# Performance work log

Measured on AMD Instinct MI355X. Metric: run time of the kernel, lower is better.

## Reference

```python
import jax, jax.numpy as jnp
import numpy as np
from jax import lax

D = 2048; H = 32; N = 64; S = 2048
LW = 64; LA = 64; LG = 128; LV = 32


def _ln(z, w, b, eps):
    m = jnp.mean(z, axis=-1, keepdims=True)
    v = jnp.var(z, axis=-1, keepdims=True)
    return (z - m) * lax.rsqrt(v + eps) * w + b


def setup_inputs():
    ks = iter(jax.random.split(jax.random.key(0), 40))
    nrm = lambda shape, s=1.0: jax.random.normal(next(ks), shape, dtype=jnp.float32) * s
    return {
        "x": nrm((1, S, D)),
        "state1": nrm((D,)),
        "state2": nrm((H, N, N), 0.1),
        "v_first": nrm((S, H, N)),
        "ln1_w": jnp.ones((D,), jnp.float32),
        "ln1_b": jnp.zeros((D,), jnp.float32),
        "x_r": nrm((D,), 0.1), "x_w": nrm((D,), 0.1), "x_k": nrm((D,), 0.1),
        "x_v": nrm((D,), 0.1), "x_a": nrm((D,), 0.1), "x_g": nrm((D,), 0.1),
        "Wr": nrm((D, D), 0.02), "Wk": nrm((D, D), 0.02),
        "Wv": nrm((D, D), 0.02), "Wo": nrm((D, D), 0.02),
        "w1": nrm((D, LW), 0.02), "w2": nrm((LW, D), 0.05), "w0": nrm((D,), 0.1),
        "a1": nrm((D, LA), 0.02), "a2": nrm((LA, D), 0.05), "a0": nrm((D,), 0.1),
        "g1": nrm((D, LG), 0.02), "g2": nrm((LG, D), 0.05),
        "v1": nrm((D, LV), 0.02), "v2": nrm((LV, D), 0.05), "v0": nrm((D,), 0.1),
        "k_k": nrm((H, N), 0.5), "k_a": nrm((H, N), 0.5), "r_k": nrm((H, N), 0.5),
        "ln_x_w": jnp.ones((D,), jnp.float32),
        "ln_x_b": jnp.zeros((D,), jnp.float32),
    }


def _forward(x, state1, state2, v_first, ln1_w, ln1_b, x_r, x_w, x_k, x_v, x_a, x_g,
             Wr, Wk, Wv, Wo, w1, w2, w0, a1, a2, a0, g1, g2, v1, v2, v0,
             k_k, k_a, r_k, ln_x_w, ln_x_b):
    last_x = x
    xn = _ln(x, ln1_w, ln1_b, 1e-5)                      # (1,S,D)
    state1_out = xn[:, -1:]
    past = jnp.concatenate([state1.reshape(1, 1, D), xn[:, :-1]], axis=1)
    sx = past - xn                                        # token-shift delta
    xr = xn + sx * x_r; xw = xn + sx * x_w; xk = xn + sx * x_k
    xv = xn + sx * x_v; xa = xn + sx * x_a; xg = xn + sx * x_g
    r = (xr @ Wr.T).reshape(S, H, N)
    k = (xk @ Wk.T).reshape(S, H, N)
    v = (xv @ Wv.T).reshape(S, H, N)
    gate = jax.nn.sigmoid(xg @ g1) @ g2                   # (1,S,D)
    a = jax.nn.sigmoid((xa @ a1) @ a2 + a0).reshape(S, H, N)
    td = jnp.tanh(xw @ w1) @ w2 + w0
    w_dec = jnp.exp(-0.606531 * jax.nn.sigmoid(td)).reshape(S, H, N)
    kk = k * k_k
    kk = kk / jnp.maximum(jnp.linalg.norm(kk, axis=-1, keepdims=True), 1e-12)
    k = k * (1.0 + (a - 1.0) * k_a)
    # layer_id != 0: residual value mixing with v_first
    v = v + (v_first - v) * jax.nn.sigmoid(((xv @ v1) @ v2 + v0).reshape(S, H, N))
    b = kk * a
    a_neg = -kk

    def step(s, inp):
        # s: (H,N,N) state; each input (H,N)
        r_t, w_t, k_t, v_t, a_t, b_t = inp
        sa = jnp.einsum('hij,hj->hi', s, a_t)
        s = s * w_t[:, None, :] + sa[:, :, None] * b_t[:, None, :] + v_t[:, :, None] * k_t[:, None, :]
        return s, jnp.einsum('hij,hj->hi', s, r_t)

    state2_out, y = lax.scan(step, state2, (r, w_dec, k, v, a_neg, b))  # y: (S,H,N)
    o = _ln(y, 1.0, 0.0, 0.00064).reshape(1, S, D)       # ln_x (default affine)
    o = o * ln_x_w + ln_x_b
    rkv = (jnp.sum(r * k * r_k, axis=-1, keepdims=True) * v).reshape(1, S, D)
    o = (o + rkv) * gate
    o = o @ Wo.T
    return last_x + o, state1_out, state2_out


def reference(x, state1, state2, v_first, ln1_w, ln1_b, x_r, x_w, x_k, x_v, x_a, x_g,
              Wr, Wk, Wv, Wo, w1, w2, w0, a1, a2, a0, g1, g2, v1, v2, v0,
              k_k, k_a, r_k, ln_x_w, ln_x_b):
    return _forward(x, state1, state2, v_first, ln1_w, ln1_b, x_r, x_w, x_k, x_v, x_a, x_g,
                    Wr, Wk, Wv, Wo, w1, w2, w0, a1, a2, a0, g1, g2, v1, v2, v0,
                    k_k, k_a, r_k, ln_x_w, ln_x_b)
```

## Files before the change

kernel.cpp:

```cpp
#include <hip/hip_runtime.h>
#include <math.h>

#define kD 2048
#define kH 32
#define kN 64
#define kS 2048

typedef unsigned short ushort_t;
typedef unsigned int uint32;

__device__ __forceinline__ ushort_t f2bf(float f) {
  uint32 u = __float_as_uint(f);
  u += 0x7fffu + ((u >> 16) & 1u);
  return (ushort_t)(u >> 16);
}
__device__ __forceinline__ float bf2f(ushort_t u) {
  return __uint_as_float(((uint32)u) << 16);
}
__device__ __forceinline__ float sigm(float x) { return 1.f / (1.f + __expf(-x)); }

__global__ __launch_bounds__(256) void ln1_kernel(
    const float* __restrict__ x, const float* __restrict__ w, const float* __restrict__ b,
    ushort_t* __restrict__ xnbf, ushort_t* __restrict__ xprevbf,
    const float* __restrict__ state1, float* __restrict__ state1_out)
// ... 64 lines not shown

__global__ __launch_bounds__(256) void gemm_bf16_b(GemmArgs args)
{
  int z = blockIdx.z;
  const ushort_t* __restrict__ A = args.A[z];
  const ushort_t* __restrict__ B = args.B[z];
  float* __restrict__ C = args.C[z];
  const float* __restrict__ resid = args.resid[z];

  __shared__ __align__(16) ushort_t As[128 * 64];
  __shared__ __align__(16) ushort_t Bs[128 * 64];
  int tid = threadIdx.x;
  int w = tid >> 6, lane = tid & 63;
  int row0 = blockIdx.y * 128, col0 = blockIdx.x * 128;
  int wrow = (w >> 1) * 64, wcol = (w & 1) * 64;
  int quad = lane >> 4, r16 = lane & 15;
  f32x4 acc[4][4] = {};

  int lrow = lane >> 3;
  int lsw  = (lane & 7) ^ lrow;

  for (int k0 = 0; k0 < kD; k0 += 64) {
    #pragma unroll
    for (int n = 0; n < 4; n++) {
      int rr = w * 32 + n * 8 + lrow;
      int cc = k0 + lsw * 8;
      const ushort_t* ga = A + (size_t)(row0 + rr) * kD + cc;
      const ushort_t* gb = B + (size_t)(col0 + rr) * kD + cc;
      __builtin_amdgcn_global_load_lds(
          (const __attribute__((address_space(1))) uint32*)ga,
          (__attribute__((address_space(3))) uint32*)&As[(w * 32 + n * 8) * 64], 16, 0, 0);
      __builtin_amdgcn_global_load_lds(
          (const __attribute__((address_space(1))) uint32*)gb,
          (__attribute__((address_space(3))) uint32*)&Bs[(w * 32 + n * 8) * 64], 16, 0, 0);
    }
    __syncthreads();
    #pragma unroll
    for (int kk = 0; kk < 64; kk += 32) {
      bf16x8 af[4], bfr[4];
      #pragma unroll
      for (int i = 0; i < 4; i++) {
        int row = wrow + i * 16 + r16;
        int chunk = ((kk >> 3) + quad) ^ (r16 & 7);
        af[i] = *(const bf16x8*)&As[row * 64 + chunk * 8];
      }
      #pragma unroll
      for (int j = 0; j < 4; j++) {
        int row = wcol + j * 16 + r16;
        int chunk = ((kk >> 3) + quad) ^ (r16 & 7);
        bfr[j] = *(const bf16x8*)&Bs[row * 64 + chunk * 8];
      }
      #pragma unroll
      for (int i = 0; i < 4; i++)
        #pragma unroll
        for (int j = 0; j < 4; j++)
          acc[i][j] = __builtin_amdgcn_mfma_f32_16x16x32_bf16(af[i], bfr[j], acc[i][j], 0, 0, 0);
    }
    __syncthreads();
  }
  #pragma unroll
  for (int i = 0; i < 4; i++) {
    #pragma unroll
    for (int j = 0; j < 4; j++) {
      int col = col0 + wcol + j * 16 + r16;
      #pragma unroll
      for (int reg = 0; reg < 4; reg++) {
        int row = row0 + wrow + i * 16 + quad * 4 + reg;
        float v = acc[i][j][reg];
        if (resid) v += resid[(size_t)row * kD + col];
        C[(size_t)row * kD + col] = v;
      }
    }
  }
}

struct PrepW1Args { const float* w1[4]; const float* c[4]; ushort_t* B1; };
__global__ __launch_bounds__(256) void prep_w1(PrepW1Args a)
{
  __shared__ float tile[64][17];
  int k0 = blockIdx.x * 64;
  int col0 = blockIdx.y * 16;
  int z, lc0, L;
  if (col0 < 128)      { z = 0; lc0 = col0;       L = 128; }
  else if (col0 < 192) { z = 1; lc0 = col0 - 128; L = 64; }
  else if (col0 < 256) { z = 2; lc0 = col0 - 192; L = 64; }
  else if (col0 < 288) { z = 3; lc0 = col0 - 256; L = 32; }
  else z = -1;
  int tid = threadIdx.x;
  if (z >= 0) {
    const float* W = a.w1[z];
    const float* C = a.c[z];
    int cc = tid & 15, kk = tid >> 4;
    #pragma unroll
    for (int i = 0; i < 4; i++) {
      int k = k0 + kk + i * 16;
      int ksrc = k & (kD - 1);
      float cv = C[ksrc];
      float sc = (k < kD) ? (1.f - cv) : cv;
      tile[kk + i * 16][cc] = W[(size_t)ksrc * L + lc0 + cc] * sc;
    }
  }
  __syncthreads();
  int kk2 = tid & 63, cc2 = tid >> 6;
  #pragma unroll
  for (int i = 0; i < 4; i++) {
    int col = col0 + cc2 * 4 + i;
    float v = (z >= 0) ? tile[kk2][cc2 * 4 + i] : 0.f;
    a.B1[(size_t)col * 4096 + k0 + kk2] = f2bf(v);
  }
}

struct PrepW2Args { const float* w2[4]; ushort_t* B2[4]; int L[4]; };
__global__ __launch_bounds__(256) void prep_w2(PrepW2Args a)
{
  __shared__ float tile[64][17];
  int z = blockIdx.z;
  int L = a.L[z];
  int l0 = blockIdx.y * 16;
  if (l0 >= L) return;
  int j0 = blockIdx.x * 64;
  int tid = threadIdx.x;
  const float* W = a.w2[z];
  ushort_t* out = a.B2[z];
  int jj = tid & 63;
  #pragma unroll
  for (int i = 0; i < 4; i++) {
    int ll = (tid >> 6) * 4 + i;
    tile[jj][ll] = W[(size_t)(l0 + ll) * kD + j0 + jj];
  }
  __syncthreads();
  int ll2 = tid & 15;
  #pragma unroll
  for (int i = 0; i < 4; i++) {
    int jj2 = (tid >> 4) + i * 16;
    out[(size_t)(j0 + jj2) * L + l0 + ll2] = f2bf(tile[jj2][ll2]);
  }
}

__global__ __launch_bounds__(256) void gemm1_kernel(
    const ushort_t* __restrict__ xnbf, const ushort_t* __restrict__ xprevbf,
    const ushort_t* __restrict__ B1, ushort_t* __restrict__ H)
{
  __shared__ __align__(16) ushort_t As[128 * 64];
  __shared__ __align__(16) ushort_t Bs[64 * 64];
  int tid = threadIdx.x;
  int w = tid >> 6, lane = tid & 63;
  int col0 = blockIdx.x * 64, row0 = blockIdx.y * 128;
  int quad = lane >> 4, r16 = lane & 15;
  f32x4 acc[2][4] = {};
  int lrow = lane >> 3;
  int lsw = (lane & 7) ^ lrow;

  for (int k0 = 0; k0 < 4096; k0 += 64) {
    const ushort_t* Abase = (k0 < kD) ? (xnbf + k0) : (xprevbf + (k0 - kD));
    #pragma unroll
    for (int n = 0; n < 4; n++) {
      int rr = w * 32 + n * 8 + lrow;
      const ushort_t* ga = Abase + (size_t)(row0 + rr) * kD + lsw * 8;
      __builtin_amdgcn_global_load_lds(
          (const __attribute__((address_space(1))) uint32*)ga,
          (__attribute__((address_space(3))) uint32*)&As[(w * 32 + n * 8) * 64], 16, 0, 0);
    }
    #pragma unroll
    for (int n = 0; n < 2; n++) {
      int rr = w * 16 + n * 8 + lrow;
      const ushort_t* gb = B1 + (size_t)(col0 + rr) * 4096 + k0 + lsw * 8;
      __builtin_amdgcn_global_load_lds(
          (const __attribute__((address_space(1))) uint32*)gb,
          (__attribute__((address_space(3))) uint32*)&Bs[(w * 16 + n * 8) * 64], 16, 0, 0);
    }
    __syncthreads();
    #pragma unroll
    for (int kk = 0; kk < 64; kk += 32) {
      bf16x8 af[2], bfr[4];
      #pragma unroll
      for (int i = 0; i < 2; i++) {
        int row = w * 32 + i * 16 + r16;
        int chunk = ((kk >> 3) + quad) ^ (r16 & 7);
        af[i] = *(const bf16x8*)&As[row * 64 + chunk * 8];
      }
      #pragma unroll
      for (int j = 0; j < 4; j++) {
        int row = j * 16 + r16;
        int chunk = ((kk >> 3) + quad) ^ (r16 & 7);
        bfr[j] = *(const bf16x8*)&Bs[row * 64 + chunk * 8];
      }
      #pragma unroll
      for (int i = 0; i < 2; i++)
        #pragma unroll
        for (int j = 0; j < 4; j++)
          acc[i][j] = __builtin_amdgcn_mfma_f32_16x16x32_bf16(af[i], bfr[j], acc[i][j], 0, 0, 0);
    }
    __syncthreads();
  }
  #pragma unroll
  for (int i = 0; i < 2; i++) {
    #pragma unroll
    for (int j = 0; j < 4; j++) {
      int col = col0 + j * 16 + r16;
      #pragma unroll
      for (int reg = 0; reg < 4; reg++) {
        int row = row0 + w * 32 + i * 16 + quad * 4 + reg;
        float v = acc[i][j][reg];
        if (col < 128) v = sigm(v);
        else if (col >= 192 && col < 256) v = tanhf(v);
        H[(size_t)row * 320 + col] = f2bf(v);
      }
    }
  }
}

struct Gemm2Args {
  const ushort_t* H;
  const ushort_t* B2[4];
  int Aofs[4];
  int L[4];
  const float* bias[4];
  float* out[4];
  const float* vfirst;
};
__global__ __launch_bounds__(256) void gemm2_kernel(Gemm2Args a)
{
  int z = blockIdx.z;
  int L = a.L[z];
  int nch = L >> 3;
  int rs = __builtin_ctz(nch);
  int mask = (nch >= 8) ? 7 : (nch - 1);
  __shared__ __align__(16) ushort_t As[128 * 128];
  __shared__ __align__(16) ushort_t Bs[128 * 128];
  int tid = threadIdx.x;
  int w = tid >> 6, lane = tid & 63;
  int row0 = blockIdx.y * 128, col0 = blockIdx.x * 128;
  int wrow = (w >> 1) * 64, wcol = (w & 1) * 64;
  int quad = lane >> 4, r16 = lane & 15;
  const ushort_t* A = a.H + a.Aofs[z];
  const ushort_t* B = a.B2[z];

  int nld = (128 * nch) >> 8;
  for (int i = 0; i < nld; i++) {
    int c = i * 256 + w * 64 + lane;
    int row = c >> rs;
    int ch = c & (nch - 1);
    int gch = ch ^ (row & mask);
    __builtin_amdgcn_global_load_lds(
        (const __attribute__((address_space(1))) uint32*)(A + (size_t)(row0 + row) * 320 + gch * 8),
        (__attribute__((address_space(3))) uint32*)&As[(i * 256 + w * 64) * 8], 16, 0, 0);
    __builtin_amdgcn_global_load_lds(
        (const __attribute__((address_space(1))) uint32*)(B + (size_t)(col0 + row) * L + gch * 8),
        (__attribute__((address_space(3))) uint32*)&Bs[(i * 256 + w * 64) * 8], 16, 0, 0);
  }
  __syncthreads();

  f32x4 acc[4][4] = {};
  int ksteps = L >> 5;
  for (int ks = 0; ks < ksteps; ks++) {
    bf16x8 af[4], bfr[4];
    #pragma unroll
    for (int i = 0; i < 4; i++) {
      int row = wrow + i * 16 + r16;
      int slot = ((ks << 2) + quad) ^ (r16 & mask);
      af[i] = *(const bf16x8*)&As[row * L + slot * 8];
    }
    #pragma unroll
    for (int j = 0; j < 4; j++) {
      int row = wcol + j * 16 + r16;
      int slot = ((ks << 2) + quad) ^ (r16 & mask);
      bfr[j] = *(const bf16x8*)&Bs[row * L + slot * 8];
    }
    #pragma unroll
    for (int i = 0; i < 4; i++)
      #pragma unroll
      for (int j = 0; j < 4; j++)
        acc[i][j] = __builtin_amdgcn_mfma_f32_16x16x32_bf16(af[i], bfr[j], acc[i][j], 0, 0, 0);
  }

  const float* bias = a.bias[z];
  float* C = a.out[z];
  #pragma unroll
  for (int i = 0; i < 4; i++) {
    #pragma unroll
    for (int j = 0; j < 4; j++) {
      int col = col0 + wcol + j * 16 + r16;
      #pragma unroll
      for (int reg = 0; reg < 4; reg++) {
        int row = row0 + wrow + i * 16 + quad * 4 + reg;
        float s = acc[i][j][reg];
        size_t idx = (size_t)row * kD + col;
        if (z == 0) {
          C[idx] = s;
        } else if (z == 1) {
          C[idx] = sigm(s + bias[col]);
        } else if (z == 2) {
          C[idx] = __expf(-0.606531f * sigm(s + bias[col]));
        } else {
          float vv = C[idx];
          C[idx] = vv + (a.vfirst[idx] - vv) * sigm(s + bias[col]);
        }
      }
    }
  }
}

__global__ __launch_bounds__(256) void post_kernel(
    float* __restrict__ kArr, float* __restrict__ kkArr, float* __restrict__ bArr,
    const float* __restrict__ aArr, float* __restrict__ rArr, const float* __restrict__ wArr,
    const float* __restrict__ k_k, const float* __restrict__ k_a, const float* __restrict__ r_k,
    float* __restrict__ c12, float* __restrict__ c3)
{
  int gid = blockIdx.x * 4 + (threadIdx.x >> 6);
  int lane = threadIdx.x & 63;
  int h = gid & (kH - 1);
  int d = h * kN + lane;
  size_t off = (size_t)gid * kN + lane;
  float kv = kArr[off];
  float kkv = kv * k_k[d];
  float ss = kkv * kkv;
  #pragma unroll
  for (int o = 32; o > 0; o >>= 1) ss += __shfl_xor(ss, o);
  float scale = 1.f / fmaxf(sqrtf(ss), 1e-12f);
  float kkf = kkv * scale;
  kkArr[off] = -kkf;
  float av = aArr[off];
  float bv = kkf * av;
  bArr[off] = bv;
  float knew = kv * (1.f + (av - 1.f) * k_a[d]);
  kArr[off] = knew;
  float rv = rArr[off];
  float wv = wArr[off];
  rArr[off] = wv * rv;
  float p1 = bv * rv;
  float p2 = knew * rv;
  float p3 = rv * knew * r_k[d];
  #pragma unroll
  for (int o = 32; o > 0; o >>= 1) {
    p1 += __shfl_xor(p1, o); p2 += __shfl_xor(p2, o); p3 += __shfl_xor(p3, o);
  }
  if (lane == 0) {
    c12[(size_t)gid * 4]     = p1;
    c12[(size_t)gid * 4 + 1] = p2;
    c3[gid] = p3;
  }
}

#define SLOT_F 344
#define NSLOT 32
#define PHASE 16

__device__ __forceinline__ void row_allsum2(float& x, float& y) {
  int t;
  t = __builtin_amdgcn_update_dpp(0, __float_as_int(x), 0x121, 0xF, 0xF, true);
  x += __int_as_float(t);
  t = __builtin_amdgcn_update_dpp(0, __float_as_int(y), 0x121, 0xF, 0xF, true);
  y += __int_as_float(t);
  t = __builtin_amdgcn_update_dpp(0, __float_as_int(x), 0x122, 0xF, 0xF, true);
  x += __int_as_float(t);
  t = __builtin_amdgcn_update_dpp(0, __float_as_int(y), 0x122, 0xF, 0xF, true);
  y += __int_as_float(t);
  t = __builtin_amdgcn_update_dpp(0, __float_as_int(x), 0x124, 0xF, 0xF, true);
  x += __int_as_float(t);
  t = __builtin_amdgcn_update_dpp(0, __float_as_int(y), 0x124, 0xF, 0xF, true);
  y += __int_as_float(t);
  t = __builtin_amdgcn_update_dpp(0, __float_as_int(x), 0x128, 0xF, 0xF, true);
  x += __int_as_float(t);
  t = __builtin_amdgcn_update_dpp(0, __float_as_int(y), 0x128, 0xF, 0xF, true);
  y += __int_as_float(t);
}

__global__ __launch_bounds__(320) void scan_kernel(
    const float* __restrict__ s0_in, const float* __restrict__ wA, const float* __restrict__ wrA,
    const float* __restrict__ kA, const float* __restrict__ vA, const float* __restrict__ kkA,
    const float* __restrict__ bA, const float* __restrict__ c12,
    float* __restrict__ y, float* __restrict__ s_out)
{
  __shared__ __align__(16) float ring[NSLOT * SLOT_F];
  int blk = blockIdx.x;
  int h = blk & 31;
  int i0 = (blk >> 5) << 4;
  int wid = threadIdx.x >> 6;
  int lane = threadIdx.x & 63;
  int hv = h * kN;

  if (wid == 0) {
    int sel = lane >> 4;
    const float* b1 = (sel == 0) ? wA : (sel == 1) ? wrA : (sel == 2) ? kA : kkA;
    b1 += hv + (lane & 15) * 4;
    const float* b2;
    size_t st2;
    if (lane < 16)      { b2 = bA + hv + lane * 4;             st2 = kD; }
    else if (lane < 20) { b2 = vA + hv + i0 + (lane - 16) * 4; st2 = kD; }
    else                { b2 = c12 + (size_t)h * 4;            st2 = kH * 4; }
    bool m2 = (lane < 21);

    #define ISSUE(t)                                                                       \
      {                                                                                    \
        float* sb = &ring[((t) & (NSLOT - 1)) * SLOT_F];                                   \
        __builtin_amdgcn_global_load_lds(                                                  \
            (const __attribute__((address_space(1))) uint32*)(b1 + (size_t)(t) * kD),      \
            (__attribute__((address_space(3))) uint32*)sb, 16, 0, 0);                      \
        if (m2)                                                                            \
          __builtin_amdgcn_global_load_lds(                                                \
              (const __attribute__((address_space(1))) uint32*)(b2 + (size_t)(t) * st2),   \
              (__attribute__((address_space(3))) uint32*)(sb + 256), 16, 0, 0);            \
      }
    for (int t = 0; t < PHASE; t++) ISSUE(t);
    __syncthreads();
    for (int ph = 0; ph < kS / PHASE; ph++) {
      int t0 = ph * PHASE + PHASE;
      if (t0 < kS) {
        for (int t = t0; t < t0 + PHASE; t++) ISSUE(t);
      }
      __syncthreads();
    }
    #undef ISSUE
  } else {
    int col16 = lane & 15;
    int row = lane >> 4;
    int vidx = (wid - 1) * 4 + row;
    int i = i0 + vidx;
    int co = col16 * 4;
    size_t srow = ((size_t)(hv + i)) * kN + co;
    float4 sS = *(const float4*)(s0_in + srow);
    float* py = y + (size_t)(hv + i);

    __syncthreads();

    float4 Aw4, Awr4, Ak4, Akk4, Ab4; float Av1, Ac1, Ac2;
    float4 Bw4, Bwr4, Bk4, Bkk4, Bb4; float Bv1, Bc1, Bc2;

    #define LOADSLOT(sl, W, WR, K, KK, B, V, C1, C2)             \
      {                                                          \
        const float* sb = &ring[(sl) * SLOT_F];                  \
        W  = *(const float4*)(sb + co);                          \
        WR = *(const float4*)(sb + 64 + co);                     \
        K  = *(const float4*)(sb + 128 + co);                    \
        KK = *(const float4*)(sb + 192 + co);                    \
        B  = *(const float4*)(sb + 256 + co);                    \
        V  = sb[320 + vidx];                                     \
        C1 = sb[336];                                            \
        C2 = sb[337];                                            \
      }
    #define STEP(W, WR, K, KK, B, V, C1, C2)                                  \
      {                                                                       \
        float sa = sS.x * KK.x + sS.y * KK.y + sS.z * KK.z + sS.w * KK.w;     \
        float u  = sS.x * WR.x + sS.y * WR.y + sS.z * WR.z + sS.w * WR.w;     \
        row_allsum2(sa, u);                                                   \
        sS.x = fmaf(sS.x, W.x, fmaf(sa, B.x, V * K.x));                       \
        sS.y = fmaf(sS.y, W.y, fmaf(sa, B.y, V * K.y));                       \
        sS.z = fmaf(sS.z, W.z, fmaf(sa, B.z, V * K.z));                       \
        sS.w = fmaf(sS.w, W.w, fmaf(sa, B.w, V * K.w));                       \
        float yv = fmaf(sa, C1, fmaf(V, C2, u));                              \
        if (col16 == 0) *py = yv;                                             \
        py += kD;                                                             \
      }

    for (int ph = 0; ph < kS / PHASE; ph++) {
      int t0 = ph * PHASE;
      LOADSLOT(t0 & (NSLOT - 1), Aw4, Awr4, Ak4, Akk4, Ab4, Av1, Ac1, Ac2);
      #pragma unroll
      for (int s = 0; s < PHASE; s += 2) {
        LOADSLOT((t0 + s + 1) & (NSLOT - 1), Bw4, Bwr4, Bk4, Bkk4, Bb4, Bv1, Bc1, Bc2);
        STEP(Aw4, Awr4, Ak4, Akk4, Ab4, Av1, Ac1, Ac2);
        if (s + 2 < PHASE)
          LOADSLOT((t0 + s + 2) & (NSLOT - 1), Aw4, Awr4, Ak4, Akk4, Ab4, Av1, Ac1, Ac2);
        STEP(Bw4, Bwr4, Bk4, Bkk4, Bb4, Bv1, Bc1, Bc2);
      }
      __syncthreads();
    }
    #undef LOADSLOT
    #undef STEP
    *(float4*)(s_out + srow) = sS;
  }
}

__global__ __launch_bounds__(256) void out_kernel(
    const float* __restrict__ y, const float* __restrict__ vA, const float* __restrict__ c3,
    const float* __restrict__ lnw, const float* __restrict__ lnb,
    const float* __restrict__ gate, ushort_t* __restrict__ Ay)
{
  int gid = blockIdx.x * 4 + (threadIdx.x >> 6);
  int lane = threadIdx.x & 63;
  int h = gid & (kH - 1);
  size_t off = (size_t)gid * kN + lane;
  float yv = y[off];
  float s = yv, s2 = yv * yv;
  #pragma unroll
  for (int o = 32; o > 0; o >>= 1) { s += __shfl_xor(s, o); s2 += __shfl_xor(s2, o); }
  float mean = s * (1.f / kN);
  float var = s2 * (1.f / kN) - mean * mean;
  float o1 = (yv - mean) * rsqrtf(var + 0.00064f);
  int d = h * kN + lane;
  float ov = o1 * lnw[d] + lnb[d];
  float rkv = c3[gid] * vA[off];
  Ay[off] = f2bf((ov + rkv) * gate[off]);
}

extern "C" void kernel_launch(void* const* d_in, const int* in_sizes, int n_in,
                              void* d_out, int out_size, void* d_ws, size_t ws_size,
                              hipStream_t stream)
{
  const float* x      = (const float*)d_in[0];
  const float* state1 = (const float*)d_in[1];
  const float* state2 = (const float*)d_in[2];
  const float* vfirst = (const float*)d_in[3];
  const float* ln1w   = (const float*)d_in[4];
  const float* ln1b   = (const float*)d_in[5];
  const float* xr_c   = (const float*)d_in[6];
  const float* xw_c   = (const float*)d_in[7];
  const float* xk_c   = (const float*)d_in[8];
  const float* xv_c   = (const float*)d_in[9];
  const float* xa_c   = (const float*)d_in[10];
  const float* xg_c   = (const float*)d_in[11];
  const float* Wr     = (const float*)d_in[12];
  const float* Wk     = (const float*)d_in[13];
  const float* Wv     = (const float*)d_in[14];
  const float* Wo     = (const float*)d_in[15];
  const float* w1     = (const float*)d_in[16];
  const float* w2     = (const float*)d_in[17];
  const float* w0     = (const float*)d_in[18];
  const float* a1     = (const float*)d_in[19];
  const float* a2     = (const float*)d_in[20];
  const float* a0     = (const float*)d_in[21];
  const float* g1     = (const float*)d_in[22];
  const float* g2     = (const float*)d_in[23];
  const float* v1     = (const float*)d_in[24];
  const float* v2     = (const float*)d_in[25];
  const float* v0     = (const float*)d_in[26];
  const float* k_k    = (const float*)d_in[27];
  const float* k_a    = (const float*)d_in[28];
  const float* r_k    = (const float*)d_in[29];
  const float* lnxw   = (const float*)d_in[30];
  const float* lnxb   = (const float*)d_in[31];

  float* out0  = (float*)d_out;
  float* s1out = out0 + (size_t)kS * kD;
  float* s2out = s1out + kD;

  size_t SD = (size_t)kS * kD;
  float* ws  = (float*)d_ws;
  float* xnB = ws;
  float* rB  = ws + SD;
  float* kB  = ws + 2 * SD;
  float* vB  = ws + 3 * SD;
  float* wB  = ws + 4 * SD;
  float* aB  = ws + 5 * SD;
  float* kkB = ws + 6 * SD;
  float* bB  = ws + 7 * SD;
  float* gB  = ws + 8 * SD;
  float* yB  = ws + 9 * SD;

  ushort_t* xnbf    = (ushort_t*)xnB;
  ushort_t* xprevbf = (ushort_t*)xnB + SD;
  ushort_t* ArB = (ushort_t*)kkB;
  ushort_t* AkB = (ushort_t*)kkB + SD;
  ushort_t* AvB = (ushort_t*)bB;
  ushort_t* B1  = (ushort_t*)bB + SD;
  ushort_t* Hbuf = B1 + (size_t)320 * 4096;
  ushort_t* B2g  = Hbuf + (size_t)2048 * 320;
  ushort_t* B2a  = B2g + (size_t)2048 * 128;
  ushort_t* B2w  = B2a + (size_t)2048 * 64;
  ushort_t* B2v  = B2w + (size_t)2048 * 64;
  ushort_t* WrB = (ushort_t*)yB;
  ushort_t* WkB = (ushort_t*)yB + SD;
  ushort_t* WvB = (ushort_t*)gB;
  ushort_t* AyB = (ushort_t*)aB;
  ushort_t* WoB = (ushort_t*)rB;
  float* c12B = xnB;
  float* c3B  = xnB + (size_t)kS * kH * 4;

  ln1_kernel<<<kS, 256, 0, stream>>>(x, ln1w, ln1b, xnbf, xprevbf, state1, s1out);
  mix3_cvt<<<kS, 256, 0, stream>>>(xnbf, xprevbf, xr_c, xk_c, xv_c, ArB, AkB, AvB);

  const int CVT_BLKS = (int)(SD / 4 / 256);
  {
    CvtArgs ca;
    ca.src[0] = Wr; ca.src[1] = Wk; ca.src[2] = Wv;
    ca.dst[0] = WrB; ca.dst[1] = WkB; ca.dst[2] = WvB;
    cvt_bf16_b<<<dim3(CVT_BLKS, 3), 256, 0, stream>>>(ca);
  }
  {
    PrepW1Args pa;
    pa.w1[0] = g1; pa.w1[1] = a1; pa.w1[2] = w1; pa.w1[3] = v1;
    pa.c[0] = xg_c; pa.c[1] = xa_c; pa.c[2] = xw_c; pa.c[3] = xv_c;
    pa.B1 = B1;
    prep_w1<<<dim3(64, 20), 256, 0, stream>>>(pa);
  }
  {
    PrepW2Args pa;
    pa.w2[0] = g2; pa.w2[1] = a2; pa.w2[2] = w2; pa.w2[3] = v2;
    pa.B2[0] = B2g; pa.B2[1] = B2a; pa.B2[2] = B2w; pa.B2[3] = B2v;
    pa.L[0] = 128; pa.L[1] = 64; pa.L[2] = 64; pa.L[3] = 32;
    prep_w2<<<dim3(32, 8, 4), 256, 0, stream>>>(pa);
  }
  {
    GemmArgs ga;
    ga.A[0] = ArB; ga.A[1] = AkB; ga.A[2] = AvB;
    ga.B[0] = WrB; ga.B[1] = WkB; ga.B[2] = WvB;
    ga.C[0] = rB;  ga.C[1] = kB;  ga.C[2] = vB;
    ga.resid[0] = nullptr; ga.resid[1] = nullptr; ga.resid[2] = nullptr;
    gemm_bf16_b<<<dim3(16, 16, 3), 256, 0, stream>>>(ga);
  }

  gemm1_kernel<<<dim3(5, 16), 256, 0, stream>>>(xnbf, xprevbf, B1, Hbuf);
  {
    Gemm2Args ga;
    ga.H = Hbuf;
    ga.B2[0] = B2g; ga.B2[1] = B2a; ga.B2[2] = B2w; ga.B2[3] = B2v;
    ga.Aofs[0] = 0; ga.Aofs[1] = 128; ga.Aofs[2] = 192; ga.Aofs[3] = 256;
    ga.L[0] = 128; ga.L[1] = 64; ga.L[2] = 64; ga.L[3] = 32;
    ga.bias[0] = nullptr; ga.bias[1] = a0; ga.bias[2] = w0; ga.bias[3] = v0;
    ga.out[0] = gB; ga.out[1] = aB; ga.out[2] = wB; ga.out[3] = vB;
    ga.vfirst = vfirst;
    gemm2_kernel<<<dim3(16, 16, 4), 256, 0, stream>>>(ga);
  }

  post_kernel<<<kS * kH / 4, 256, 0, stream>>>(kB, kkB, bB, aB, rB, wB,
                                               k_k, k_a, r_k, c12B, c3B);

  scan_kernel<<<kH * 4, 320, 0, stream>>>(state2, wB, rB, kB, vB, kkB, bB, c12B, yB, s2out);

  out_kernel<<<kS * kH / 4, 256, 0, stream>>>(yB, vB, c3B, lnxw, lnxb, gB, AyB);

  {
    CvtArgs ca;
    ca.src[0] = Wo; ca.src[1] = Wo; ca.src[2] = Wo;
    ca.dst[0] = WoB; ca.dst[1] = WoB; ca.dst[2] = WoB;
    cvt_bf16_b<<<dim3(CVT_BLKS, 1), 256, 0, stream>>>(ca);
  }
  {
    GemmArgs ga;
    ga.A[0] = AyB; ga.A[1] = AyB; ga.A[2] = AyB;
    ga.B[0] = WoB; ga.B[1] = WoB; ga.B[2] = WoB;
    ga.C[0] = out0; ga.C[1] = out0; ga.C[2] = out0;
    ga.resid[0] = x; ga.resid[1] = x; ga.resid[2] = x;
    gemm_bf16_b<<<dim3(16, 16, 1), 256, 0, stream>>>(ga);
  }
}
```

Before: 736.5 us.

## Replace LDS-ring scan producer with packed-record register prefetch pipeline

The scan kernel drops its dedicated producer wave and the LDS ring filled by global_load_lds. All four waves now load their per-step operands straight from global memory into registers, keeping four steps of prefetch in flight. post_kernel writes k, -kk and b into one packed per-(t,h) record, stops writing w*r back to memory (the scan computes it), and halves the c12 stride. The workspace layout is reshuffled to match, and the output buffer now holds the gate as scratch. The aim is to remove LDS round-trips and block-wide barriers from the serial recurrence and to cut post_kernel write traffic. The cost is that global-load latency is now hidden only by the 4-deep register prefetch, and the last iterations prefetch past the end of the arrays.

```diff
diff --git a/kernel.cpp b/kernel.cpp
--- a/kernel.cpp
+++ b/kernel.cpp
@@ -390,10 +390,10 @@
 }
 
 __global__ __launch_bounds__(256) void post_kernel(
-    float* __restrict__ kArr, float* __restrict__ kkArr, float* __restrict__ bArr,
-    const float* __restrict__ aArr, float* __restrict__ rArr, const float* __restrict__ wArr,
+    const float* __restrict__ kArr, const float* __restrict__ aArr,
+    const float* __restrict__ rArr, const float* __restrict__ wArr,
     const float* __restrict__ k_k, const float* __restrict__ k_a, const float* __restrict__ r_k,
-    float* __restrict__ c12, float* __restrict__ c3)
+    float* __restrict__ PACK, float* __restrict__ c12, float* __restrict__ c3)
 {
   int gid = blockIdx.x * 4 + (threadIdx.x >> 6);
   int lane = threadIdx.x & 63;
@@ -407,15 +407,14 @@
   for (int o = 32; o > 0; o >>= 1) ss += __shfl_xor(ss, o);
   float scale = 1.f / fmaxf(sqrtf(ss), 1e-12f);
   float kkf = kkv * scale;
-  kkArr[off] = -kkf;
   float av = aArr[off];
   float bv = kkf * av;
-  bArr[off] = bv;
   float knew = kv * (1.f + (av - 1.f) * k_a[d]);
-  kArr[off] = knew;
+  float* rec = PACK + (size_t)gid * 192;
+  rec[lane]       = knew;
+  rec[64 + lane]  = -kkf;
+  rec[128 + lane] = bv;
   float rv = rArr[off];
-  float wv = wArr[off];
-  rArr[off] = wv * rv;
   float p1 = bv * rv;
   float p2 = knew * rv;
   float p3 = rv * knew * r_k[d];
@@ -424,15 +423,11 @@
     p1 += __shfl_xor(p1, o); p2 += __shfl_xor(p2, o); p3 += __shfl_xor(p3, o);
   }
   if (lane == 0) {
-    c12[(size_t)gid * 4]     = p1;
-    c12[(size_t)gid * 4 + 1] = p2;
+    c12[(size_t)gid * 2]     = p1;
+    c12[(size_t)gid * 2 + 1] = p2;
     c3[gid] = p3;
   }
 }
-
-#define SLOT_F 344
-#define NSLOT 32
-#define PHASE 16
 
 __device__ __forceinline__ void row_allsum2(float& x, float& y) {
   int t;
@@ -454,110 +449,75 @@
   y += __int_as_float(t);
 }
 
-__global__ __launch_bounds__(320) void scan_kernel(
-    const float* __restrict__ s0_in, const float* __restrict__ wA, const float* __restrict__ wrA,
-    const float* __restrict__ kA, const float* __restrict__ vA, const float* __restrict__ kkA,
-    const float* __restrict__ bA, const float* __restrict__ c12,
+struct ScanBuf { float4 k4, kk4, b4, w4, r4; float v1, c1, c2; };
+
+__global__ __launch_bounds__(256) void scan_kernel(
+    const float* __restrict__ s0_in, const float* __restrict__ PACK,
+    const float* __restrict__ wA, const float* __restrict__ rA,
+    const float* __restrict__ vA, const float* __restrict__ c12,
     float* __restrict__ y, float* __restrict__ s_out)
 {
-  __shared__ __align__(16) float ring[NSLOT * SLOT_F];
   int blk = blockIdx.x;
   int h = blk & 31;
   int i0 = (blk >> 5) << 4;
   int wid = threadIdx.x >> 6;
   int lane = threadIdx.x & 63;
+  int col16 = lane & 15;
+  int row = lane >> 4;
+  int vidx = wid * 4 + row;
+  int i = i0 + vidx;
+  int co = col16 * 4;
   int hv = h * kN;
 
-  if (wid == 0) {
-    int sel = lane >> 4;
-    const float* b1 = (sel == 0) ? wA : (sel == 1) ? wrA : (sel == 2) ? kA : kkA;
-    b1 += hv + (lane & 15) * 4;
-    const float* b2;
-    size_t st2;
-    if (lane < 16)      { b2 = bA + hv + lane * 4;             st2 = kD; }
-    else if (lane < 20) { b2 = vA + hv + i0 + (lane - 16) * 4; st2 = kD; }
-    else                { b2 = c12 + (size_t)h * 4;            st2 = kH * 4; }
-    bool m2 = (lane < 21);
-
-    #define ISSUE(t)                                                                       \
-      {                                                                                    \
-        float* sb = &ring[((t) & (NSLOT - 1)) * SLOT_F];                                   \
-        __builtin_amdgcn_global_load_lds(                                                  \
-            (const __attribute__((address_space(1))) uint32*)(b1 + (size_t)(t) * kD),      \
-            (__attribute__((address_space(3))) uint32*)sb, 16, 0, 0);                      \
-        if (m2)                                                                            \
-          __builtin_amdgcn_global_load_lds(                                                \
-              (const __attribute__((address_space(1))) uint32*)(b2 + (size_t)(t) * st2),   \
-              (__attribute__((address_space(3))) uint32*)(sb + 256), 16, 0, 0);            \
-      }
-    for (int t = 0; t < PHASE; t++) ISSUE(t);
-    __syncthreads();
-    for (int ph = 0; ph < kS / PHASE; ph++) {
-      int t0 = ph * PHASE + PHASE;
-      if (t0 < kS) {
-        for (int t = t0; t < t0 + PHASE; t++) ISSUE(t);
-      }
-      __syncthreads();
-    }
-    #undef ISSUE
-  } else {
-    int col16 = lane & 15;
-    int row = lane >> 4;
-    int vidx = (wid - 1) * 4 + row;
-    int i = i0 + vidx;
-    int co = col16 * 4;
-    size_t srow = ((size_t)(hv + i)) * kN + co;
-    float4 sS = *(const float4*)(s0_in + srow);
-    float* py = y + (size_t)(hv + i);
-
-    __syncthreads();
-
-    float4 Aw4, Awr4, Ak4, Akk4, Ab4; float Av1, Ac1, Ac2;
-    float4 Bw4, Bwr4, Bk4, Bkk4, Bb4; float Bv1, Bc1, Bc2;
-
-    #define LOADSLOT(sl, W, WR, K, KK, B, V, C1, C2)             \
-      {                                                          \
-        const float* sb = &ring[(sl) * SLOT_F];                  \
-        W  = *(const float4*)(sb + co);                          \
-        WR = *(const float4*)(sb + 64 + co);                     \
-        K  = *(const float4*)(sb + 128 + co);                    \
-        KK = *(const float4*)(sb + 192 + co);                    \
-        B  = *(const float4*)(sb + 256 + co);                    \
-        V  = sb[320 + vidx];                                     \
-        C1 = sb[336];                                            \
-        C2 = sb[337];                                            \
-      }
-    #define STEP(W, WR, K, KK, B, V, C1, C2)                                  \
-      {                                                                       \
-        float sa = sS.x * KK.x + sS.y * KK.y + sS.z * KK.z + sS.w * KK.w;     \
-        float u  = sS.x * WR.x + sS.y * WR.y + sS.z * WR.z + sS.w * WR.w;     \
-        row_allsum2(sa, u);                                                   \
-        sS.x = fmaf(sS.x, W.x, fmaf(sa, B.x, V * K.x));                       \
-        sS.y = fmaf(sS.y, W.y, fmaf(sa, B.y, V * K.y));                       \
-        sS.z = fmaf(sS.z, W.z, fmaf(sa, B.z, V * K.z));                       \
-        sS.w = fmaf(sS.w, W.w, fmaf(sa, B.w, V * K.w));                       \
-        float yv = fmaf(sa, C1, fmaf(V, C2, u));                              \
-        if (col16 == 0) *py = yv;                                             \
-        py += kD;                                                             \
-      }
-
-    for (int ph = 0; ph < kS / PHASE; ph++) {
-      int t0 = ph * PHASE;
-      LOADSLOT(t0 & (NSLOT - 1), Aw4, Awr4, Ak4, Akk4, Ab4, Av1, Ac1, Ac2);
-      #pragma unroll
-      for (int s = 0; s < PHASE; s += 2) {
-        LOADSLOT((t0 + s + 1) & (NSLOT - 1), Bw4, Bwr4, Bk4, Bkk4, Bb4, Bv1, Bc1, Bc2);
-        STEP(Aw4, Awr4, Ak4, Akk4, Ab4, Av1, Ac1, Ac2);
-        if (s + 2 < PHASE)
-          LOADSLOT((t0 + s + 2) & (NSLOT - 1), Aw4, Awr4, Ak4, Akk4, Ab4, Av1, Ac1, Ac2);
-        STEP(Bw4, Bwr4, Bk4, Bkk4, Bb4, Bv1, Bc1, Bc2);
-      }
-      __syncthreads();
-    }
-    #undef LOADSLOT
-    #undef STEP
-    *(float4*)(s_out + srow) = sS;
-  }
+  size_t srow = ((size_t)(hv + i)) * kN + co;
+  float4 sS = *(const float4*)(s0_in + srow);
+  float* py = y + (size_t)(hv + i);
+
+  const float* rec = PACK + (size_t)h * 192 + co;
+  const float* wp  = wA + hv + co;
+  const float* rp  = rA + hv + co;
+  const float* vp  = vA + hv + i;
+  const float* cp  = c12 + (size_t)h * 2;
+
+  #define ISSUE(B, t)                                              \
+    {                                                              \
+      const float* rb = rec + (size_t)(t) * 6144;                  \
+      B.k4  = *(const float4*)(rb);                                \
+      B.kk4 = *(const float4*)(rb + 64);                           \
+      B.b4  = *(const float4*)(rb + 128);                          \
+      B.w4  = *(const float4*)(wp + (size_t)(t) * kD);             \
+      B.r4  = *(const float4*)(rp + (size_t)(t) * kD);             \
+      B.v1  = vp[(size_t)(t) * kD];                                \
+      float2 cc = *(const float2*)(cp + (size_t)(t) * 64);         \
+      B.c1 = cc.x; B.c2 = cc.y;                                    \
+    }
+  #define STEP(B)                                                               \
+    {                                                                           \
+      float wrx = B.w4.x * B.r4.x, wry = B.w4.y * B.r4.y;                       \
+      float wrz = B.w4.z * B.r4.z, wrw = B.w4.w * B.r4.w;                       \
+      float sa = sS.x * B.kk4.x + sS.y * B.kk4.y + sS.z * B.kk4.z + sS.w * B.kk4.w; \
+      float u  = sS.x * wrx + sS.y * wry + sS.z * wrz + sS.w * wrw;             \
+      row_allsum2(sa, u);                                                       \
+      sS.x = fmaf(sS.x, B.w4.x, fmaf(sa, B.b4.x, B.v1 * B.k4.x));               \
+      sS.y = fmaf(sS.y, B.w4.y, fmaf(sa, B.b4.y, B.v1 * B.k4.y));               \
+      sS.z = fmaf(sS.z, B.w4.z, fmaf(sa, B.b4.z, B.v1 * B.k4.z));               \
+      sS.w = fmaf(sS.w, B.w4.w, fmaf(sa, B.b4.w, B.v1 * B.k4.w));               \
+      float yv = fmaf(sa, B.c1, fmaf(B.v1, B.c2, u));                           \
+      if (col16 == 0) *py = yv;                                                 \
+      py += kD;                                                                 \
+    }
+
+  ScanBuf b0, b1, b2, b3;
+  ISSUE(b0, 0); ISSUE(b1, 1); ISSUE(b2, 2); ISSUE(b3, 3);
+  for (int t = 0; t < kS; t += 4) {
+    STEP(b0); ISSUE(b0, t + 4);
+    STEP(b1); ISSUE(b1, t + 5);
+    STEP(b2); ISSUE(b2, t + 6);
+    STEP(b3); ISSUE(b3, t + 7);
+  }
+  #undef ISSUE
+  #undef STEP
+  *(float4*)(s_out + srow) = sS;
 }
 
 __global__ __launch_bounds__(256) void out_kernel(
@@ -625,35 +585,36 @@
 
   size_t SD = (size_t)kS * kD;
   float* ws  = (float*)d_ws;
-  float* xnB = ws;
+  float* vB  = ws;
   float* rB  = ws + SD;
   float* kB  = ws + 2 * SD;
-  float* vB  = ws + 3 * SD;
-  float* wB  = ws + 4 * SD;
-  float* aB  = ws + 5 * SD;
-  float* kkB = ws + 6 * SD;
-  float* bB  = ws + 7 * SD;
-  float* gB  = ws + 8 * SD;
-  float* yB  = ws + 9 * SD;
-
-  ushort_t* xnbf    = (ushort_t*)xnB;
-  ushort_t* xprevbf = (ushort_t*)xnB + SD;
-  ushort_t* ArB = (ushort_t*)kkB;
-  ushort_t* AkB = (ushort_t*)kkB + SD;
-  ushort_t* AvB = (ushort_t*)bB;
-  ushort_t* B1  = (ushort_t*)bB + SD;
+  float* wB  = ws + 3 * SD;
+  float* aB  = ws + 4 * SD;
+  float* xyB = ws + 5 * SD;
+  float* PK  = ws + 6 * SD;
+  float* s9  = ws + 9 * SD;
+
+  ushort_t* xnbf    = (ushort_t*)xyB;
+  ushort_t* xprevbf = (ushort_t*)xyB + SD;
+  float*    yB      = xyB;
+
+  ushort_t* ArB = (ushort_t*)PK;
+  ushort_t* AkB = ArB + SD;
+  ushort_t* AvB = AkB + SD;
+  ushort_t* B1  = AvB + SD;
   ushort_t* Hbuf = B1 + (size_t)320 * 4096;
   ushort_t* B2g  = Hbuf + (size_t)2048 * 320;
   ushort_t* B2a  = B2g + (size_t)2048 * 128;
   ushort_t* B2w  = B2a + (size_t)2048 * 64;
   ushort_t* B2v  = B2w + (size_t)2048 * 64;
-  ushort_t* WrB = (ushort_t*)yB;
-  ushort_t* WkB = (ushort_t*)yB + SD;
-  ushort_t* WvB = (ushort_t*)gB;
-  ushort_t* AyB = (ushort_t*)aB;
+  ushort_t* WrB = (ushort_t*)wB;
+  ushort_t* WkB = (ushort_t*)wB + SD;
+  ushort_t* WvB = (ushort_t*)aB;
+  ushort_t* AyB = (ushort_t*)kB;
   ushort_t* WoB = (ushort_t*)rB;
-  float* c12B = xnB;
-  float* c3B  = xnB + (size_t)kS * kH * 4;
+  float* gB = out0;
+  float* c12B = s9;
+  float* c3B  = s9 + (size_t)kS * kH * 2;
 
   ln1_kernel<<<kS, 256, 0, stream>>>(x, ln1w, ln1b, xnbf, xprevbf, state1, s1out);
   mix3_cvt<<<kS, 256, 0, stream>>>(xnbf, xprevbf, xr_c, xk_c, xv_c, ArB, AkB, AvB);
@@ -701,10 +662,10 @@
     gemm2_kernel<<<dim3(16, 16, 4), 256, 0, stream>>>(ga);
   }
 
-  post_kernel<<<kS * kH / 4, 256, 0, stream>>>(kB, kkB, bB, aB, rB, wB,
-                                               k_k, k_a, r_k, c12B, c3B);
-
-  scan_kernel<<<kH * 4, 320, 0, stream>>>(state2, wB, rB, kB, vB, kkB, bB, c12B, yB, s2out);
+  post_kernel<<<kS * kH / 4, 256, 0, stream>>>(kB, aB, rB, wB,
+                                               k_k, k_a, r_k, PK, c12B, c3B);
+
+  scan_kernel<<<kH * 4, 256, 0, stream>>>(state2, PK, wB, rB, vB, c12B, yB, s2out);
 
   out_kernel<<<kS * kH / 4, 256, 0, stream>>>(yB, vB, c3B, lnxw, lnxb, gB, AyB);
 
```

New measurement: 933.7 us. 1.27x slower.

## Deepen scan LDS ring pipeline with partial vmcnt waits and register prefetch

Applied to the files above, without the earlier changes.

The producer wave now issues two phases of global-to-LDS loads ahead. Instead of a full __syncthreads drain, it waits only until the older phase has landed (s_waitcnt vmcnt(16)) and then uses a raw s_barrier. The phase length drops to 8 and the ring to 24 slots, and the consumer waves keep a 4-deep rotating register prefetch of slot contents across phase boundaries. The goal is to keep the serial recurrence from stalling on memory latency and barrier drains, but prefetching into the next phase before its loads are guaranteed complete risks a race.

```diff
diff --git a/kernel.cpp b/kernel.cpp
--- a/kernel.cpp
+++ b/kernel.cpp
@@ -431,8 +431,8 @@
 }
 
 #define SLOT_F 344
-#define NSLOT 32
-#define PHASE 16
+#define NSLOT 24
+#define PHASE 8
 
 __device__ __forceinline__ void row_allsum2(float& x, float& y) {
   int t;
@@ -454,6 +454,8 @@
   y += __int_as_float(t);
 }
 
+struct SBuf { float4 W, WR, K, KK, Bb; float V, C1, C2; };
+
 __global__ __launch_bounds__(320) void scan_kernel(
     const float* __restrict__ s0_in, const float* __restrict__ wA, const float* __restrict__ wrA,
     const float* __restrict__ kA, const float* __restrict__ vA, const float* __restrict__ kkA,
@@ -479,9 +481,10 @@
     else                { b2 = c12 + (size_t)h * 4;            st2 = kH * 4; }
     bool m2 = (lane < 21);
 
+    int slot = 0;
     #define ISSUE(t)                                                                       \
       {                                                                                    \
-        float* sb = &ring[((t) & (NSLOT - 1)) * SLOT_F];                                   \
+        float* sb = &ring[slot * SLOT_F];                                                  \
         __builtin_amdgcn_global_load_lds(                                                  \
             (const __attribute__((address_space(1))) uint32*)(b1 + (size_t)(t) * kD),      \
             (__attribute__((address_space(3))) uint32*)sb, 16, 0, 0);                      \
@@ -489,15 +492,22 @@
           __builtin_amdgcn_global_load_lds(                                                \
               (const __attribute__((address_space(1))) uint32*)(b2 + (size_t)(t) * st2),   \
               (__attribute__((address_space(3))) uint32*)(sb + 256), 16, 0, 0);            \
-      }
-    for (int t = 0; t < PHASE; t++) ISSUE(t);
-    __syncthreads();
+        slot++; if (slot == NSLOT) slot = 0;                                               \
+      }
+    for (int t = 0; t < 2 * PHASE; t++) ISSUE(t);
+    asm volatile("s_waitcnt vmcnt(16)" ::: "memory");
+    __builtin_amdgcn_sched_barrier(0);
+    __builtin_amdgcn_s_barrier();
     for (int ph = 0; ph < kS / PHASE; ph++) {
-      int t0 = ph * PHASE + PHASE;
+      int t0 = ph * PHASE + 2 * PHASE;
       if (t0 < kS) {
         for (int t = t0; t < t0 + PHASE; t++) ISSUE(t);
-      }
-      __syncthreads();
+        asm volatile("s_waitcnt vmcnt(16)" ::: "memory");
+      } else {
+        asm volatile("s_waitcnt vmcnt(0)" ::: "memory");
+      }
+      __builtin_amdgcn_sched_barrier(0);
+      __builtin_amdgcn_s_barrier();
     }
     #undef ISSUE
   } else {
@@ -510,50 +520,49 @@
     float4 sS = *(const float4*)(s0_in + srow);
     float* py = y + (size_t)(hv + i);
 
-    __syncthreads();
-
-    float4 Aw4, Awr4, Ak4, Akk4, Ab4; float Av1, Ac1, Ac2;
-    float4 Bw4, Bwr4, Bk4, Bkk4, Bb4; float Bv1, Bc1, Bc2;
-
-    #define LOADSLOT(sl, W, WR, K, KK, B, V, C1, C2)             \
+    #define LOADSLOT(sl, S)                                      \
       {                                                          \
         const float* sb = &ring[(sl) * SLOT_F];                  \
-        W  = *(const float4*)(sb + co);                          \
-        WR = *(const float4*)(sb + 64 + co);                     \
-        K  = *(const float4*)(sb + 128 + co);                    \
-        KK = *(const float4*)(sb + 192 + co);                    \
-        B  = *(const float4*)(sb + 256 + co);                    \
-        V  = sb[320 + vidx];                                     \
-        C1 = sb[336];                                            \
-        C2 = sb[337];                                            \
-      }
-    #define STEP(W, WR, K, KK, B, V, C1, C2)                                  \
+        S.W  = *(const float4*)(sb + co);                        \
+        S.WR = *(const float4*)(sb + 64 + co);                   \
+        S.K  = *(const float4*)(sb + 128 + co);                  \
+        S.KK = *(const float4*)(sb + 192 + co);                  \
+        S.Bb = *(const float4*)(sb + 256 + co);                  \
+        S.V  = sb[320 + vidx];                                   \
+        S.C1 = sb[336];                                          \
+        S.C2 = sb[337];                                          \
+      }
+    #define STEP(S)                                                           \
       {                                                                       \
-        float sa = sS.x * KK.x + sS.y * KK.y + sS.z * KK.z + sS.w * KK.w;     \
-        float u  = sS.x * WR.x + sS.y * WR.y + sS.z * WR.z + sS.w * WR.w;     \
+        float sa = sS.x * S.KK.x + sS.y * S.KK.y + sS.z * S.KK.z + sS.w * S.KK.w; \
+        float u  = sS.x * S.WR.x + sS.y * S.WR.y + sS.z * S.WR.z + sS.w * S.WR.w; \
         row_allsum2(sa, u);                                                   \
-        sS.x = fmaf(sS.x, W.x, fmaf(sa, B.x, V * K.x));                       \
-        sS.y = fmaf(sS.y, W.y, fmaf(sa, B.y, V * K.y));                       \
-        sS.z = fmaf(sS.z, W.z, fmaf(sa, B.z, V * K.z));                       \
-        sS.w = fmaf(sS.w, W.w, fmaf(sa, B.w, V * K.w));                       \
-        float yv = fmaf(sa, C1, fmaf(V, C2, u));                              \
+        sS.x = fmaf(sS.x, S.W.x, fmaf(sa, S.Bb.x, S.V * S.K.x));              \
+        sS.y = fmaf(sS.y, S.W.y, fmaf(sa, S.Bb.y, S.V * S.K.y));              \
+        sS.z = fmaf(sS.z, S.W.z, fmaf(sa, S.Bb.z, S.V * S.K.z));              \
+        sS.w = fmaf(sS.w, S.W.w, fmaf(sa, S.Bb.w, S.V * S.K.w));              \
+        float yv = fmaf(sa, S.C1, fmaf(S.V, S.C2, u));                        \
         if (col16 == 0) *py = yv;                                             \
         py += kD;                                                             \
       }
 
+    __builtin_amdgcn_s_barrier();
+    SBuf q0, q1, q2, q3;
+    LOADSLOT(0, q0); LOADSLOT(1, q1); LOADSLOT(2, q2); LOADSLOT(3, q3);
+    int rs = 4;
+    #define PF(S) { LOADSLOT(rs, S); rs++; if (rs == NSLOT) rs = 0; }
     for (int ph = 0; ph < kS / PHASE; ph++) {
-      int t0 = ph * PHASE;
-      LOADSLOT(t0 & (NSLOT - 1), Aw4, Awr4, Ak4, Akk4, Ab4, Av1, Ac1, Ac2);
-      #pragma unroll
-      for (int s = 0; s < PHASE; s += 2) {
-        LOADSLOT((t0 + s + 1) & (NSLOT - 1), Bw4, Bwr4, Bk4, Bkk4, Bb4, Bv1, Bc1, Bc2);
-        STEP(Aw4, Awr4, Ak4, Akk4, Ab4, Av1, Ac1, Ac2);
-        if (s + 2 < PHASE)
-          LOADSLOT((t0 + s + 2) & (NSLOT - 1), Aw4, Awr4, Ak4, Akk4, Ab4, Av1, Ac1, Ac2);
-        STEP(Bw4, Bwr4, Bk4, Bkk4, Bb4, Bv1, Bc1, Bc2);
-      }
-      __syncthreads();
-    }
+      STEP(q0); PF(q0);
+      STEP(q1); PF(q1);
+      STEP(q2); PF(q2);
+      STEP(q3); PF(q3);
+      STEP(q0); PF(q0);
+      STEP(q1); PF(q1);
+      STEP(q2); PF(q2);
+      STEP(q3); PF(q3);
+      __builtin_amdgcn_s_barrier();
+    }
+    #undef PF
     #undef LOADSLOT
     #undef STEP
     *(float4*)(s_out + srow) = sS;
```

New measurement: 753.7 us. 1.02x slower.

## Drop dedicated producer wave in scan; compute waves stage own prefetch

Applied to the files above, without the earlier changes.

The scan kernel previously used a separate producer wavefront that issued global-to-LDS loads while four compute waves ran the recurrence. Now all four waves split the staging of the next phase between them, using a double-buffered ring with explicit waitcnt and s_barrier, and the block shrinks from 320 to 256 threads. This removes the extra wave and its barrier coupling and lets prefetch overlap compute inside each wave. The cost is that staging instructions now sit in the critical serial path of every compute wave, and the hand-tuned vmcnt(16) count must match the number of loads each wave has in flight.

```diff
diff --git a/kernel.cpp b/kernel.cpp
--- a/kernel.cpp
+++ b/kernel.cpp
@@ -454,7 +454,9 @@
   y += __int_as_float(t);
 }
 
-__global__ __launch_bounds__(320) void scan_kernel(
+struct SBuf { float4 W, WR, K, KK, Bb; float V, C1, C2; };
+
+__global__ __launch_bounds__(256) void scan_kernel(
     const float* __restrict__ s0_in, const float* __restrict__ wA, const float* __restrict__ wrA,
     const float* __restrict__ kA, const float* __restrict__ vA, const float* __restrict__ kkA,
     const float* __restrict__ bA, const float* __restrict__ c12,
@@ -468,96 +470,100 @@
   int lane = threadIdx.x & 63;
   int hv = h * kN;
 
-  if (wid == 0) {
-    int sel = lane >> 4;
-    const float* b1 = (sel == 0) ? wA : (sel == 1) ? wrA : (sel == 2) ? kA : kkA;
-    b1 += hv + (lane & 15) * 4;
-    const float* b2;
-    size_t st2;
-    if (lane < 16)      { b2 = bA + hv + lane * 4;             st2 = kD; }
-    else if (lane < 20) { b2 = vA + hv + i0 + (lane - 16) * 4; st2 = kD; }
-    else                { b2 = c12 + (size_t)h * 4;            st2 = kH * 4; }
-    bool m2 = (lane < 21);
-
-    #define ISSUE(t)                                                                       \
-      {                                                                                    \
-        float* sb = &ring[((t) & (NSLOT - 1)) * SLOT_F];                                   \
-        __builtin_amdgcn_global_load_lds(                                                  \
-            (const __attribute__((address_space(1))) uint32*)(b1 + (size_t)(t) * kD),      \
-            (__attribute__((address_space(3))) uint32*)sb, 16, 0, 0);                      \
-        if (m2)                                                                            \
-          __builtin_amdgcn_global_load_lds(                                                \
-              (const __attribute__((address_space(1))) uint32*)(b2 + (size_t)(t) * st2),   \
-              (__attribute__((address_space(3))) uint32*)(sb + 256), 16, 0, 0);            \
-      }
-    for (int t = 0; t < PHASE; t++) ISSUE(t);
-    __syncthreads();
-    for (int ph = 0; ph < kS / PHASE; ph++) {
-      int t0 = ph * PHASE + PHASE;
-      if (t0 < kS) {
-        for (int t = t0; t < t0 + PHASE; t++) ISSUE(t);
-      }
-      __syncthreads();
-    }
-    #undef ISSUE
-  } else {
-    int col16 = lane & 15;
-    int row = lane >> 4;
-    int vidx = (wid - 1) * 4 + row;
-    int i = i0 + vidx;
-    int co = col16 * 4;
-    size_t srow = ((size_t)(hv + i)) * kN + co;
-    float4 sS = *(const float4*)(s0_in + srow);
-    float* py = y + (size_t)(hv + i);
-
-    __syncthreads();
-
-    float4 Aw4, Awr4, Ak4, Akk4, Ab4; float Av1, Ac1, Ac2;
-    float4 Bw4, Bwr4, Bk4, Bkk4, Bb4; float Bv1, Bc1, Bc2;
-
-    #define LOADSLOT(sl, W, WR, K, KK, B, V, C1, C2)             \
-      {                                                          \
-        const float* sb = &ring[(sl) * SLOT_F];                  \
-        W  = *(const float4*)(sb + co);                          \
-        WR = *(const float4*)(sb + 64 + co);                     \
-        K  = *(const float4*)(sb + 128 + co);                    \
-        KK = *(const float4*)(sb + 192 + co);                    \
-        B  = *(const float4*)(sb + 256 + co);                    \
-        V  = sb[320 + vidx];                                     \
-        C1 = sb[336];                                            \
-        C2 = sb[337];                                            \
-      }
-    #define STEP(W, WR, K, KK, B, V, C1, C2)                                  \
-      {                                                                       \
-        float sa = sS.x * KK.x + sS.y * KK.y + sS.z * KK.z + sS.w * KK.w;     \
-        float u  = sS.x * WR.x + sS.y * WR.y + sS.z * WR.z + sS.w * WR.w;     \
-        row_allsum2(sa, u);                                                   \
-        sS.x = fmaf(sS.x, W.x, fmaf(sa, B.x, V * K.x));                       \
-        sS.y = fmaf(sS.y, W.y, fmaf(sa, B.y, V * K.y));                       \
-        sS.z = fmaf(sS.z, W.z, fmaf(sa, B.z, V * K.z));                       \
-        sS.w = fmaf(sS.w, W.w, fmaf(sa, B.w, V * K.w));                       \
-        float yv = fmaf(sa, C1, fmaf(V, C2, u));                              \
-        if (col16 == 0) *py = yv;                                             \
-        py += kD;                                                             \
-      }
-
-    for (int ph = 0; ph < kS / PHASE; ph++) {
-      int t0 = ph * PHASE;
-      LOADSLOT(t0 & (NSLOT - 1), Aw4, Awr4, Ak4, Akk4, Ab4, Av1, Ac1, Ac2);
-      #pragma unroll
-      for (int s = 0; s < PHASE; s += 2) {
-        LOADSLOT((t0 + s + 1) & (NSLOT - 1), Bw4, Bwr4, Bk4, Bkk4, Bb4, Bv1, Bc1, Bc2);
-        STEP(Aw4, Awr4, Ak4, Akk4, Ab4, Av1, Ac1, Ac2);
-        if (s + 2 < PHASE)
-          LOADSLOT((t0 + s + 2) & (NSLOT - 1), Aw4, Awr4, Ak4, Akk4, Ab4, Av1, Ac1, Ac2);
-        STEP(Bw4, Bwr4, Bk4, Bkk4, Bb4, Bv1, Bc1, Bc2);
-      }
-      __syncthreads();
-    }
-    #undef LOADSLOT
-    #undef STEP
-    *(float4*)(s_out + srow) = sS;
-  }
+  int sel = lane >> 4;
+  const float* b1 = (sel == 0) ? wA : (sel == 1) ? wrA : (sel == 2) ? kA : kkA;
+  b1 += hv + (lane & 15) * 4;
+  const float* b2;
+  size_t st2;
+  if (lane < 16)      { b2 = bA + hv + lane * 4;             st2 = kD; }
+  else if (lane < 20) { b2 = vA + hv + i0 + (lane - 16) * 4; st2 = kD; }
+  else                { b2 = c12 + (size_t)h * 4;            st2 = kH * 4; }
+  bool m2 = (lane < 21);
+
+  int col16 = lane & 15;
+  int row = lane >> 4;
+  int vidx = wid * 4 + row;
+  int i = i0 + vidx;
+  int co = col16 * 4;
+  size_t srow = ((size_t)(hv + i)) * kN + co;
+  float4 sS = *(const float4*)(s0_in + srow);
+  float* py = y + (size_t)(hv + i);
+
+  #define STAGE(t, slot)                                                                 \
+    {                                                                                    \
+      float* sb = &ring[(slot) * SLOT_F];                                                \
+      __builtin_amdgcn_global_load_lds(                                                  \
+          (const __attribute__((address_space(1))) uint32*)(b1 + (size_t)(t) * kD),      \
+          (__attribute__((address_space(3))) uint32*)sb, 16, 0, 0);                      \
+      if (m2)                                                                            \
+        __builtin_amdgcn_global_load_lds(                                                \
+            (const __attribute__((address_space(1))) uint32*)(b2 + (size_t)(t) * st2),   \
+            (__attribute__((address_space(3))) uint32*)(sb + 256), 16, 0, 0);            \
+    }
+
+  #define LOADSLOT(slot, S)                                      \
+    {                                                            \
+      const float* sb = &ring[(slot) * SLOT_F];                  \
+      S.W  = *(const float4*)(sb + co);                          \
+      S.WR = *(const float4*)(sb + 64 + co);                     \
+      S.K  = *(const float4*)(sb + 128 + co);                    \
+      S.KK = *(const float4*)(sb + 192 + co);                    \
+      S.Bb = *(const float4*)(sb + 256 + co);                    \
+      S.V  = sb[320 + vidx];                                     \
+      float2 cc = *(const float2*)(sb + 336);                    \
+      S.C1 = cc.x; S.C2 = cc.y;                                  \
+    }
+  #define STEP(S)                                                                 \
+    {                                                                             \
+      float sa = sS.x * S.KK.x + sS.y * S.KK.y + sS.z * S.KK.z + sS.w * S.KK.w;   \
+      float u  = sS.x * S.WR.x + sS.y * S.WR.y + sS.z * S.WR.z + sS.w * S.WR.w;   \
+      row_allsum2(sa, u);                                                         \
+      sS.x = fmaf(sS.x, S.W.x, fmaf(sa, S.Bb.x, S.V * S.K.x));                    \
+      sS.y = fmaf(sS.y, S.W.y, fmaf(sa, S.Bb.y, S.V * S.K.y));                    \
+      sS.z = fmaf(sS.z, S.W.z, fmaf(sa, S.Bb.z, S.V * S.K.z));                    \
+      sS.w = fmaf(sS.w, S.W.w, fmaf(sa, S.Bb.w, S.V * S.K.w));                    \
+      float yv = fmaf(sa, S.C1, fmaf(S.V, S.C2, u));                              \
+      if (col16 == 0) *py = yv;                                                   \
+      py += kD;                                                                   \
+    }
+
+  SBuf qA, qB;
+
+  #define HALFPHASE(T0, BASE)                                                    \
+    {                                                                            \
+      if ((T0) + PHASE < kS) {                                                   \
+        for (int s = wid; s < PHASE; s += 4) STAGE((T0) + PHASE + s, ((BASE) ^ 16) + s); \
+      }                                                                          \
+      __builtin_amdgcn_sched_barrier(0);                                         \
+      LOADSLOT((BASE) + 0, qA);                                                  \
+      _Pragma("unroll")                                                          \
+      for (int s = 0; s < PHASE; s += 2) {                                       \
+        LOADSLOT((BASE) + s + 1, qB);                                            \
+        STEP(qA);                                                                \
+        if (s + 2 < PHASE) LOADSLOT((BASE) + s + 2, qA);                         \
+        STEP(qB);                                                                \
+      }                                                                          \
+      asm volatile("s_waitcnt vmcnt(16)" ::: "memory");                          \
+      __builtin_amdgcn_sched_barrier(0);                                         \
+      __builtin_amdgcn_s_barrier();                                              \
+    }
+
+  for (int s = wid; s < PHASE; s += 4) STAGE(s, s);
+  asm volatile("s_waitcnt vmcnt(0)" ::: "memory");
+  __builtin_amdgcn_sched_barrier(0);
+  __builtin_amdgcn_s_barrier();
+
+  for (int pp = 0; pp < kS / (2 * PHASE); pp++) {
+    int t0a = pp * 2 * PHASE;
+    HALFPHASE(t0a, 0)
+    HALFPHASE(t0a + PHASE, 16)
+  }
+  #undef HALFPHASE
+  #undef STEP
+  #undef LOADSLOT
+  #undef STAGE
+
+  *(float4*)(s_out + srow) = sS;
 }
 
 __global__ __launch_bounds__(256) void out_kernel(
@@ -704,7 +710,7 @@
   post_kernel<<<kS * kH / 4, 256, 0, stream>>>(kB, kkB, bB, aB, rB, wB,
                                                k_k, k_a, r_k, c12B, c3B);
 
-  scan_kernel<<<kH * 4, 320, 0, stream>>>(state2, wB, rB, kB, vB, kkB, bB, c12B, yB, s2out);
+  scan_kernel<<<kH * 4, 256, 0, stream>>>(state2, wB, rB, kB, vB, kkB, bB, c12B, yB, s2out);
 
   out_kernel<<<kS * kH / 4, 256, 0, stream>>>(yB, vB, c3B, lnxw, lnxb, gB, AyB);
 
```

Result: slower. 802.0 us (+8.9%).
